# Kernel tuning notes

Measured on AMD Instinct MI355X. Metric: run time of the kernel, lower is better.

## Reference

```python
import jax, jax.numpy as jnp
import numpy as np

N = 50000      # nodes
E = 800000     # edges (avg degree 16)
D_IN = 18      # 3 fields x 6 timesteps
H = 128        # hidden_dim
HEADS = 4
DH = H // HEADS
D_OUT = 3
NEG = 0.2      # LeakyReLU slope
BN_EPS = 1e-5


def leaky(x):
    return jnp.where(x >= 0, x, NEG * x)


def segment_softmax(e, row, n):
    # numerically stable softmax over edges grouped by target node (axis 0)
    m = jax.ops.segment_max(e, row, num_segments=n)
    ex = jnp.exp(e - m[row])
    s = jax.ops.segment_sum(ex, row, num_segments=n)
    return ex / (s[row] + 1e-16)


def single_head_attn(x, row, col, Wv, b, a_src, a_dst):
    h = x @ Wv + b                                   # [N,H] values
    s_src = x @ a_src                                # [N] query scalar (dim=1)
    s_dst = x @ a_dst                                # [N] key scalar
    e = leaky(s_src[row] + s_dst[col])               # [E]
    alpha = segment_softmax(e, row, N)               # [E]
    return jax.ops.segment_sum(alpha[:, None] * h[col], row, num_segments=N)


def multi_head_attn(x, row, col, Wv, b, a_src, a_dst):
    h = jnp.einsum('nd,hde->nhe', x, Wv) + b         # [N,4,32] per-head values
    s_src = x @ a_src.T                              # [N,4] per-head Q (dim=1)
    s_dst = x @ a_dst.T                              # [N,4] per-head K (dim=1)
    e = leaky(s_src[row] + s_dst[col])               # [E,4]
    alpha = segment_softmax(e, row, N)               # [E,4]
    out = jax.ops.segment_sum(alpha[:, :, None] * h[col], row, num_segments=N)
    return out.reshape(N, HEADS * DH)                # concat heads -> [N,128]


def batch_norm_eval(x, g, bt, m, v):
    return (x - m) * jax.lax.rsqrt(v + BN_EPS) * g + bt


def setup_inputs() -> dict:
    key = jax.random.key(0)
    ks = jax.random.split(key, 16)
    rn = lambda k, shp, s=0.05: jax.random.normal(k, shp, dtype=jnp.float32) * s
    return {
        'x': rn(ks[0], (N, D_IN), 1.0),
        'edge_index': jax.random.randint(ks[1], (2, E), 0, N, dtype=jnp.int32),
        'W_in': rn(ks[2], (D_IN, H)),
        'b_in': jnp.zeros((H,), jnp.float32),
        'W_agg': rn(ks[3], (D_IN, H)),
        'b_agg': jnp.zeros((H,), jnp.float32),
        'sh_Wv': rn(ks[4], (2, H, H)),
        'sh_b': jnp.zeros((2, H), jnp.float32),
        'sh_asrc': rn(ks[5], (2, H)),
        'sh_adst': rn(ks[6], (2, H)),
        'mh_Wv': rn(ks[7], (HEADS, H, DH)),
        'mh_b': jnp.zeros((HEADS, DH), jnp.float32),
        'mh_asrc': rn(ks[8], (HEADS, H)),
        'mh_adst': rn(ks[9], (HEADS, H)),
        'bn_gamma': jnp.ones((3, H), jnp.float32),
        'bn_beta': jnp.zeros((3, H), jnp.float32),
        'bn_mean': jnp.zeros((3, H), jnp.float32),
        'bn_var': jnp.ones((3, H), jnp.float32),
        'W_o1': rn(ks[10], (H, H)),
        'b_o1': jnp.zeros((H,), jnp.float32),
        'W_o2': rn(ks[11], (H, D_OUT), 0.01),
        'b_o2': jnp.zeros((D_OUT,), jnp.float32),
    }


def reference(x, edge_index, W_in, b_in, W_agg, b_agg, sh_Wv, sh_b, sh_asrc, sh_adst,
              mh_Wv, mh_b, mh_asrc, mh_adst, bn_gamma, bn_beta, bn_mean, bn_var,
              W_o1, b_o1, W_o2, b_o2):
    row, col = edge_index[0], edge_index[1]

    # explicit neighbor mean aggregation (fused gather-scatter)
    nsum = jax.ops.segment_sum(x[col], row, num_segments=N)     # [N,D_IN]
    deg = jax.ops.segment_sum(jnp.ones((E,), x.dtype), row, num_segments=N)
    nmean = nsum / (deg[:, None] + 1e-8)

    h = (x @ W_in + b_in) + (nmean @ W_agg + b_agg)             # [N,H]
    x0 = h

    # layer 0: single-head attention + BN + residual(x0) + leaky
    h1 = single_head_attn(h, row, col, sh_Wv[0], sh_b[0], sh_asrc[0], sh_adst[0])
    h1 = batch_norm_eval(h1, bn_gamma[0], bn_beta[0], bn_mean[0], bn_var[0])
    h = leaky(x0 + h1)

    # layer 1: multi-head (4 heads, Q/K dim=1) + BN, no residual (i=1), leaky
    h2 = multi_head_attn(h, row, col, mh_Wv, mh_b, mh_asrc, mh_adst)
    h2 = batch_norm_eval(h2, bn_gamma[1], bn_beta[1], bn_mean[1], bn_var[1])
    h = leaky(h2)

    # layer 2: single-head + BN + residual + leaky
    r = h
    h3 = single_head_attn(h, row, col, sh_Wv[1], sh_b[1], sh_asrc[1], sh_adst[1])
    h3 = batch_norm_eval(h3, bn_gamma[2], bn_beta[2], bn_mean[2], bn_var[2])
    h = leaky(r + h3)

    # output head (dropout is a no-op in eval)
    delta = leaky(h @ W_o1 + b_o1) @ W_o2 + b_o2                # [N,3]

    # residual skip from last timestep of the input sequence
    return x[:, -D_OUT:] + delta
```

## Files before the change

kernel.cpp:

```cpp
#include <hip/hip_runtime.h>
#include <math.h>

#define DIN 18
#define HID 128
#define NEGS 0.2f
#define BN_EPS 1e-5f
#define SCHUNK 2048

typedef unsigned short ushort_t;
typedef __attribute__((ext_vector_type(8))) short bf16x8;
typedef __attribute__((ext_vector_type(4))) float f32x4;

__device__ __forceinline__ float leaky(float x){ return x >= 0.f ? x : NEGS * x; }

__device__ __forceinline__ float wred_sum(float v){
  #pragma unroll
  for (int off = 32; off; off >>= 1) v += __shfl_xor(v, off);
  return v;
}

__device__ __forceinline__ ushort_t f2bf(float f){
  union { float f; unsigned u; } v; v.f = f;
  unsigned r = v.u + 0x7FFFu + ((v.u >> 16) & 1u);
  return (ushort_t)(r >> 16);
}
__device__ __forceinline__ float bf_lo(unsigned p){ return __uint_as_float(p << 16); }
__device__ __forceinline__ float bf_hi(unsigned p){ return __uint_as_float(p & 0xFFFF0000u); }
__device__ __forceinline__ unsigned packbf(float a, float b){
  return (unsigned)f2bf(a) | ((unsigned)f2bf(b) << 16);
}

__device__ __forceinline__ float sel4(float v0, float v1, float v2, float v3, int hd){
  float a = (hd & 1) ? v1 : v0;
  float b = (hd & 1) ? v3 : v2;
  return (hd & 2) ? b : a;
}

__global__ void k_deg_rank(const int* __restrict__ row, int* __restrict__ deg,
                           int* __restrict__ rank, int E){
  int i = blockIdx.x * blockDim.x + threadIdx.x;
  if (i < E) rank[i] = atomicAdd(&deg[row[i]], 1);
}

__global__ void k_scan1(const int* __restrict__ deg, int* __restrict__ bsum, int n){
  __shared__ int wtot[4];
  int tid = threadIdx.x, lane = tid & 63, wid = tid >> 6;
  int base = blockIdx.x * SCHUNK + tid * 8;
  int acc = 0;
  #pragma unroll
  for (int j = 0; j < 8; ++j){
    int i = base + j;
    if (i < n) acc += deg[i];
  }
  #pragma unroll
  for (int off = 32; off; off >>= 1) acc += __shfl_xor(acc, off);
  if (lane == 0) wtot[wid] = acc;
  __syncthreads();
  if (tid == 0) bsum[blockIdx.x] = wtot[0] + wtot[1] + wtot[2] + wtot[3];
}

__global__ void k_scan2(int* __restrict__ bsum, int nb){
  int lane = threadIdx.x;
  int carry = 0;
  for (int base = 0; base < nb; base += 64){
    int i = base + lane;
    int v = (i < nb) ? bsum[i] : 0;
    #pragma unroll
    for (int off = 1; off < 64; off <<= 1){
      int u = __shfl_up(v, off);
      if (lane >= off) v += u;
    }
    if (i < nb) bsum[i] = v + carry;
    carry += __shfl(v, 63);
  }
}

__global__ void k_scan3(const int* __restrict__ deg, const int* __restrict__ bsum,
                        int* __restrict__ rowptr, int n){
  __shared__ int wtot[4];
  int tid = threadIdx.x, lane = tid & 63, wid = tid >> 6;
  int base = blockIdx.x * SCHUNK + tid * 8;
  int l[8];
  int acc = 0;
  #pragma unroll
  for (int j = 0; j < 8; ++j){
    int i = base + j;
    acc += (i < n) ? deg[i] : 0;
    l[j] = acc;
  }
  int v = acc;
  #pragma unroll
  for (int off = 1; off < 64; off <<= 1){
    int u = __shfl_up(v, off);
    if (lane >= off) v += u;
  }
  if (lane == 63) wtot[wid] = v;
  __syncthreads();
  int woff = 0;
  for (int w = 0; w < wid; ++w) woff += wtot[w];
  int boff = (blockIdx.x == 0) ? 0 : bsum[blockIdx.x - 1];
  int tpre = boff + woff + (v - acc);
  #pragma unroll
  for (int j = 0; j < 8; ++j){
    int i = base + j;
    if (i < n) rowptr[i + 1] = tpre + l[j];
  }
  if (blockIdx.x == 0 && tid == 0) rowptr[0] = 0;
}

__global__ void k_scatter(const int* __restrict__ row, const int* __restrict__ col,
                          const int* __restrict__ rowptr, const int* __restrict__ rank,
                          int* __restrict__ cols_s, int E){
  int i = blockIdx.x * blockDim.x + threadIdx.x;
  if (i < E){
    cols_s[rowptr[row[i]] + rank[i]] = col[i];
  }
}

__global__ void k_nmean(const float* __restrict__ x, const int* __restrict__ rowptr,
                        const int* __restrict__ cols, float* __restrict__ nmean, int n){
  __shared__ int s_cv[4][64];
  int wid = threadIdx.x >> 6;
  int node = blockIdx.x * 4 + wid;
  if (node >= n) return;
  int lane = threadIdx.x & 63;
  int s = rowptr[node], e = rowptr[node + 1];
  float acc = 0.f;
  for (int j0 = s; j0 < e; j0 += 64){
    int len = min(64, e - j0);
    int cv = (lane < len) ? cols[j0 + lane] : 0;
    s_cv[wid][lane] = cv;
    int k = 0;
    for (; k + 8 <= len; k += 8){
      float p[8];
      #pragma unroll
      for (int u = 0; u < 8; ++u){
        int c = s_cv[wid][k + u];
        p[u] = (lane < DIN) ? x[c * DIN + lane] : 0.f;
      }
      #pragma unroll
      for (int u = 0; u < 8; ++u) acc += p[u];
    }
    for (; k < len; ++k){
      int c = s_cv[wid][k];
      if (lane < DIN) acc += x[c * DIN + lane];
    }
  }
  if (lane < DIN){
    float d = (float)(e - s);
    nmean[node * DIN + lane] = acc / (d + 1e-8f);
  }
}

__global__ void k_h_in(const float* __restrict__ x, const float* __restrict__ nmean,
                       const float* __restrict__ Win, const float* __restrict__ bin,
                       const float* __restrict__ Wagg, const float* __restrict__ bagg,
                       const float* __restrict__ asrc, const float* __restrict__ adst,
                       float* __restrict__ ssrc, float* __restrict__ sdst,
                       ushort_t* __restrict__ out, int n){
  int wid = threadIdx.x >> 6;
  int node = blockIdx.x * 4 + wid;
  if (node >= n) return;
  int lane = threadIdx.x & 63;
  float xv = 0.f;
  if (lane < DIN) xv = x[node * DIN + lane];
  else if (lane < 2 * DIN) xv = nmean[node * DIN + (lane - DIN)];
  float acc0 = bin[lane]      + bagg[lane];
  float acc1 = bin[64 + lane] + bagg[64 + lane];
  #pragma unroll
  for (int d = 0; d < DIN; ++d){
    float xd = __shfl(xv, d);
    float nd = __shfl(xv, DIN + d);
    acc0 += xd * Win[d * HID + lane]       + nd * Wagg[d * HID + lane];
    acc1 += xd * Win[d * HID + 64 + lane]  + nd * Wagg[d * HID + 64 + lane];
  }
  out[node * HID + lane]      = f2bf(acc0);
  out[node * HID + 64 + lane] = f2bf(acc1);
  float ps = acc0 * asrc[lane] + acc1 * asrc[64 + lane];
  float pd = acc0 * adst[lane] + acc1 * adst[64 + lane];
  ps = wred_sum(ps);
  pd = wred_sum(pd);
  if (lane == 0){ ssrc[node] = ps; sdst[node] = pd; }
}

__global__ void k_wt_sh(const float* __restrict__ W, ushort_t* __restrict__ Wt){
  int i = blockIdx.x * 256 + threadIdx.x;
  int c = i >> 7, d = i & 127;
  Wt[c * HID + d] = f2bf(W[d * HID + c]);
}
__global__ void k_wt_mh(const float* __restrict__ mhWv, ushort_t* __restrict__ Wt){
  int i = blockIdx.x * 256 + threadIdx.x;
  int c = i >> 7, d = i & 127;
  Wt[c * HID + d] = f2bf(mhWv[((c >> 5) * HID + d) * 32 + (c & 31)]);
}

__global__ void k_gemm_mfma(const ushort_t* __restrict__ A, const ushort_t* __restrict__ Bt,
                            const float* __restrict__ bias, ushort_t* __restrict__ dstb,
                            int n){
  int wv = threadIdx.x >> 6, lane = threadIdx.x & 63;
  int r0 = blockIdx.x * 64 + wv * 16;
  int lr = lane & 15, lk = lane >> 4;
  int arow = r0 + lr; if (arow >= n) arow = n - 1;
  const ushort_t* Ap = A + (size_t)arow * HID + lk * 8;
  bf16x8 a[4];
  #pragma unroll
  for (int kb = 0; kb < 4; ++kb) a[kb] = *(const bf16x8*)(Ap + kb * 32);
  f32x4 acc[8];
  #pragma unroll
  for (int t = 0; t < 8; ++t) acc[t] = (f32x4){0.f, 0.f, 0.f, 0.f};
  #pragma unroll
  for (int t = 0; t < 8; ++t){
    const ushort_t* Bp = Bt + (size_t)(t * 16 + lr) * HID + lk * 8;
    #pragma unroll
    for (int kb = 0; kb < 4; ++kb){
      bf16x8 b = *(const bf16x8*)(Bp + kb * 32);
      acc[t] = __builtin_amdgcn_mfma_f32_16x16x32_bf16(a[kb], b, acc[t], 0, 0, 0);
    }
  }
  #pragma unroll
  for (int t = 0; t < 8; ++t){
    int col = t * 16 + lr;
    float bs = bias[col];
    #pragma unroll
    for (int j = 0; j < 4; ++j){
      int rr = r0 + lk * 4 + j;
      if (rr < n) dstb[(size_t)rr * HID + col] = f2bf(acc[t][j] + bs);
    }
  }
}

__global__ void k_gemm_out(const ushort_t* __restrict__ A, const ushort_t* __restrict__ Bt,
                           const float* __restrict__ bias, const float* __restrict__ Wo2,
                           const float* __restrict__ bo2, const float* __restrict__ x,
                           float* __restrict__ out, int n){
  int wv = threadIdx.x >> 6, lane = threadIdx.x & 63;
  int r0 = blockIdx.x * 64 + wv * 16;
  int lr = lane & 15, lk = lane >> 4;
  int arow = r0 + lr; if (arow >= n) arow = n - 1;
  const ushort_t* Ap = A + (size_t)arow * HID + lk * 8;
  bf16x8 a[4];
  #pragma unroll
  for (int kb = 0; kb < 4; ++kb) a[kb] = *(const bf16x8*)(Ap + kb * 32);
  f32x4 acc[8];
  #pragma unroll
  for (int t = 0; t < 8; ++t) acc[t] = (f32x4){0.f, 0.f, 0.f, 0.f};
  #pragma unroll
  for (int t = 0; t < 8; ++t){
    const ushort_t* Bp = Bt + (size_t)(t * 16 + lr) * HID + lk * 8;
    #pragma unroll
    for (int kb = 0; kb < 4; ++kb){
      bf16x8 b = *(const bf16x8*)(Bp + kb * 32);
      acc[t] = __builtin_amdgcn_mfma_f32_16x16x32_bf16(a[kb], b, acc[t], 0, 0, 0);
    }
  }
  #pragma unroll
  for (int j = 0; j < 4; ++j){
    float p0 = 0.f, p1 = 0.f, p2 = 0.f;
    #pragma unroll
    for (int t = 0; t < 8; ++t){
      int col = t * 16 + lr;
      float v = leaky(acc[t][j] + bias[col]);
      p0 += v * Wo2[col * 3 + 0];
      p1 += v * Wo2[col * 3 + 1];
      p2 += v * Wo2[col * 3 + 2];
    }
    #pragma unroll
    for (int off = 1; off < 16; off <<= 1){
      p0 += __shfl_xor(p0, off);
      p1 += __shfl_xor(p1, off);
      p2 += __shfl_xor(p2, off);
    }
    int rr = r0 + lk * 4 + j;
    if (lr == 0 && rr < n){
      out[rr * 3 + 0] = x[rr * DIN + 15] + p0 + bo2[0];
      out[rr * 3 + 1] = x[rr * DIN + 16] + p1 + bo2[1];
      out[rr * 3 + 2] = x[rr * DIN + 17] + p2 + bo2[2];
    }
  }
}

__global__ void k_agg_sh(const int* __restrict__ rowptr, const int* __restrict__ cols,
                         const float* __restrict__ ssrc, const float* __restrict__ sdst,
                         const ushort_t* __restrict__ hv, const ushort_t* __restrict__ resid,
                         const float* __restrict__ bng, const float* __restrict__ bnb,
                         const float* __restrict__ bnm, const float* __restrict__ bnv,
                         const float* __restrict__ masrc, const float* __restrict__ madst,
                         float* __restrict__ ossrc, float* __restrict__ osdst,
                         ushort_t* __restrict__ out, int n){
  __shared__ int   s_cv[4][64];
  __shared__ float s_ex[4][64];
  int wid = threadIdx.x >> 6;
  int node = blockIdx.x * 4 + wid;
  if (node >= n) return;
  int lane = threadIdx.x & 63;
  const unsigned* hv32 = (const unsigned*)hv;
  int s = rowptr[node], e = rowptr[node + 1];
  float sq = ssrc[node];
  float ssum = 0.f, a0 = 0.f, a1 = 0.f;
  for (int j0 = s; j0 < e; j0 += 64){
    int len = min(64, e - j0);
    int cv = 0; float ex = 0.f;
    if (lane < len){
      cv = cols[j0 + lane];
      ex = __expf(leaky(sq + sdst[cv]));
    }
    ssum += ex;
    s_cv[wid][lane] = cv;
    s_ex[wid][lane] = ex;
    int k = 0;
    for (; k + 16 <= len; k += 16){
      unsigned p[16]; float l[16];
      #pragma unroll
      for (int u = 0; u < 16; ++u){
        int c = s_cv[wid][k + u];
        l[u] = s_ex[wid][k + u];
        p[u] = hv32[c * 64 + lane];
      }
      #pragma unroll
      for (int u = 0; u < 16; ++u){
        a0 += l[u] * bf_lo(p[u]); a1 += l[u] * bf_hi(p[u]);
      }
    }
    for (; k + 8 <= len; k += 8){
      unsigned p[8]; float l[8];
      #pragma unroll
      for (int u = 0; u < 8; ++u){
        int c = s_cv[wid][k + u];
        l[u] = s_ex[wid][k + u];
        p[u] = hv32[c * 64 + lane];
      }
      #pragma unroll
      for (int u = 0; u < 8; ++u){
        a0 += l[u] * bf_lo(p[u]); a1 += l[u] * bf_hi(p[u]);
      }
    }
    for (; k + 4 <= len; k += 4){
      unsigned p[4]; float l[4];
      #pragma unroll
      for (int u = 0; u < 4; ++u){
        int c = s_cv[wid][k + u];
        l[u] = s_ex[wid][k + u];
        p[u] = hv32[c * 64 + lane];
      }
      #pragma unroll
      for (int u = 0; u < 4; ++u){
        a0 += l[u] * bf_lo(p[u]); a1 += l[u] * bf_hi(p[u]);
      }
    }
    for (; k < len; ++k){
      int c = s_cv[wid][k];
      float l = s_ex[wid][k];
      unsigned p = hv32[c * 64 + lane];
      a0 += l * bf_lo(p); a1 += l * bf_hi(p);
    }
  }
  ssum = wred_sum(ssum);
  float inv = 1.f / (ssum + 1e-16f);
  a0 *= inv; a1 *= inv;
  int d0 = 2 * lane, d1 = 2 * lane + 1;
  float v0 = (a0 - bnm[d0]) * rsqrtf(bnv[d0] + BN_EPS) * bng[d0] + bnb[d0];
  float v1 = (a1 - bnm[d1]) * rsqrtf(bnv[d1] + BN_EPS) * bng[d1] + bnb[d1];
  if (resid){
    unsigned rv = *(const unsigned*)&resid[node * HID + d0];
    v0 += bf_lo(rv); v1 += bf_hi(rv);
  }
  float o0 = leaky(v0), o1 = leaky(v1);
  *(unsigned*)&out[node * HID + d0] = packbf(o0, o1);
  if (ossrc){
    #pragma unroll
    for (int h = 0; h < 4; ++h){
      float ps = o0 * masrc[h * HID + d0] + o1 * masrc[h * HID + d1];
      float pd = o0 * madst[h * HID + d0] + o1 * madst[h * HID + d1];
      ps = wred_sum(ps);
      pd = wred_sum(pd);
      if (lane == 0){ ossrc[node * 4 + h] = ps; osdst[node * 4 + h] = pd; }
    }
  }
}

__global__ void k_agg_mh(const int* __restrict__ rowptr, const int* __restrict__ cols,
                         const float* __restrict__ ssrc, const float* __restrict__ sdst,
                         const ushort_t* __restrict__ hv,
                         const float* __restrict__ bng, const float* __restrict__ bnb,
                         const float* __restrict__ bnm, const float* __restrict__ bnv,
                         const float* __restrict__ sasrc, const float* __restrict__ sadst,
                         float* __restrict__ ossrc, float* __restrict__ osdst,
                         ushort_t* __restrict__ out, int n){
  __shared__ int    s_cv[4][64];
  __shared__ float4 s_ex[4][64];
  int wid = threadIdx.x >> 6;
  int node = blockIdx.x * 4 + wid;
  if (node >= n) return;
  int lane = threadIdx.x & 63;
  const unsigned* hv32 = (const unsigned*)hv;
  int s = rowptr[node], e = rowptr[node + 1];
  const float4 sq = *(const float4*)&ssrc[node * 4];
  int hd = lane >> 4;
  float s0 = 0.f, s1 = 0.f, s2 = 0.f, s3 = 0.f;
  float a0 = 0.f, a1 = 0.f;
  const float* exw = &s_ex[wid][0].x;
  for (int j0 = s; j0 < e; j0 += 64){
    int len = min(64, e - j0);
    int cv = 0;
    float e0 = 0.f, e1 = 0.f, e2 = 0.f, e3 = 0.f;
    if (lane < len){
      cv = cols[j0 + lane];
      float4 kd = *(const float4*)&sdst[cv * 4];
      e0 = __expf(leaky(sq.x + kd.x)); e1 = __expf(leaky(sq.y + kd.y));
      e2 = __expf(leaky(sq.z + kd.z)); e3 = __expf(leaky(sq.w + kd.w));
    }
    s0 += e0; s1 += e1; s2 += e2; s3 += e3;
    s_cv[wid][lane] = cv;
    s_ex[wid][lane] = make_float4(e0, e1, e2, e3);
    int k = 0;
    for (; k + 16 <= len; k += 16){
      unsigned p[16]; float l[16];
      #pragma unroll
      for (int u = 0; u < 16; ++u){
        int c = s_cv[wid][k + u];
        l[u] = exw[(k + u) * 4 + hd];
        p[u] = hv32[c * 64 + lane];
      }
      #pragma unroll
      for (int u = 0; u < 16; ++u){
        a0 += l[u] * bf_lo(p[u]); a1 += l[u] * bf_hi(p[u]);
      }
    }
    for (; k + 8 <= len; k += 8){
      unsigned p[8]; float l[8];
      #pragma unroll
      for (int u = 0; u < 8; ++u){
        int c = s_cv[wid][k + u];
        l[u] = exw[(k + u) * 4 + hd];
        p[u] = hv32[c * 64 + lane];
      }
      #pragma unroll
      for (int u = 0; u < 8; ++u){
        a0 += l[u] * bf_lo(p[u]); a1 += l[u] * bf_hi(p[u]);
      }
    }
    for (; k + 4 <= len; k += 4){
      unsigned p[4]; float l[4];
      #pragma unroll
      for (int u = 0; u < 4; ++u){
        int c = s_cv[wid][k + u];
        l[u] = exw[(k + u) * 4 + hd];
        p[u] = hv32[c * 64 + lane];
      }
      #pragma unroll
      for (int u = 0; u < 4; ++u){
        a0 += l[u] * bf_lo(p[u]); a1 += l[u] * bf_hi(p[u]);
      }
    }
    for (; k < len; ++k){
      int c = s_cv[wid][k];
      float l = exw[k * 4 + hd];
      unsigned p = hv32[c * 64 + lane];
      a0 += l * bf_lo(p); a1 += l * bf_hi(p);
    }
  }
  s0 = wred_sum(s0); s1 = wred_sum(s1);
  s2 = wred_sum(s2); s3 = wred_sum(s3);
  float i0 = 1.f / (s0 + 1e-16f), i1 = 1.f / (s1 + 1e-16f);
  float i2 = 1.f / (s2 + 1e-16f), i3 = 1.f / (s3 + 1e-16f);
  float ih = sel4(i0, i1, i2, i3, hd);
  a0 *= ih; a1 *= ih;
  int d0 = 2 * lane, d1 = 2 * lane + 1;
  float v0 = (a0 - bnm[d0]) * rsqrtf(bnv[d0] + BN_EPS) * bng[d0] + bnb[d0];
  float v1 = (a1 - bnm[d1]) * rsqrtf(bnv[d1] + BN_EPS) * bng[d1] + bnb[d1];
  float o0 = leaky(v0), o1 = leaky(v1);
  *(unsigned*)&out[node * HID + d0] = packbf(o0, o1);
  float ps = o0 * sasrc[d0] + o1 * sasrc[d1];
  float pd = o0 * sadst[d0] + o1 * sadst[d1];
  ps = wred_sum(ps);
  pd = wred_sum(pd);
  if (lane == 0){ ossrc[node] = ps; osdst[node] = pd; }
}

extern "C" void kernel_launch(void* const* d_in, const int* in_sizes, int n_in,
                              void* d_out, int out_size, void* d_ws, size_t ws_size,
                              hipStream_t stream){
  const float* x       = (const float*)d_in[0];
  const int*   ei      = (const int*)  d_in[1];
  const float* W_in    = (const float*)d_in[2];
  const float* b_in    = (const float*)d_in[3];
  const float* W_agg   = (const float*)d_in[4];
  const float* b_agg   = (const float*)d_in[5];
  const float* sh_Wv   = (const float*)d_in[6];
  const float* sh_b    = (const float*)d_in[7];
  const float* sh_asrc = (const float*)d_in[8];
  const float* sh_adst = (const float*)d_in[9];
  const float* mh_Wv   = (const float*)d_in[10];
  const float* mh_b    = (const float*)d_in[11];
  const float* mh_asrc = (const float*)d_in[12];
  const float* mh_adst = (const float*)d_in[13];
  const float* bn_g    = (const float*)d_in[14];
  const float* bn_bt   = (const float*)d_in[15];
  const float* bn_m    = (const float*)d_in[16];
  const float* bn_v    = (const float*)d_in[17];
  const float* W_o1    = (const float*)d_in[18];
  const float* b_o1    = (const float*)d_in[19];
  const float* W_o2    = (const float*)d_in[20];
  const float* b_o2    = (const float*)d_in[21];
  float* out = (float*)d_out;

  const int N = in_sizes[0] / DIN;
  const int E = in_sizes[1] / 2;
  const int* row = ei;
  const int* col = ei + E;

  char* w = (char*)d_ws;
  size_t off = 0;
  auto alloc = [&](size_t bytes) -> void* {
    void* p = w + off;
    off = (off + bytes + 255) & ~(size_t)255;
    return p;
  };
  int*      tmp    = (int*)     alloc((size_t)N * 4);
  int*      rowptr = (int*)     alloc((size_t)(N + 1) * 4);
  int*      cols_s = (int*)     alloc((size_t)E * 4);
  int*      rank   = (int*)     alloc((size_t)E * 4);
  int*      bsum   = (int*)     alloc((size_t)1024 * 4);
  float*    nmean  = (float*)   alloc((size_t)N * DIN * 4);
  float*    ssrcA  = (float*)   alloc((size_t)N * 4);
  float*    sdstA  = (float*)   alloc((size_t)N * 4);
  float*    ssrcB  = (float*)   alloc((size_t)N * 4 * 4);
  float*    sdstB  = (float*)   alloc((size_t)N * 4 * 4);
  ushort_t* wt0    = (ushort_t*)alloc((size_t)HID * HID * 2);
  ushort_t* wt1    = (ushort_t*)alloc((size_t)HID * HID * 2);
  ushort_t* wt2    = (ushort_t*)alloc((size_t)HID * HID * 2);
  ushort_t* wt3    = (ushort_t*)alloc((size_t)HID * HID * 2);
  ushort_t* b0     = (ushort_t*)alloc((size_t)N * HID * 2);
  ushort_t* b1     = (ushort_t*)alloc((size_t)N * HID * 2);
  ushort_t* hvb    = (ushort_t*)alloc((size_t)N * HID * 2);

  const int eb = (E + 255) / 256;
  const int nb4 = (N + 3) / 4;
  const int gb = (N + 63) / 64;
  const int nsb = (N + SCHUNK - 1) / SCHUNK;

  hipMemsetAsync(tmp, 0, (size_t)N * 4, stream);
  k_deg_rank<<<eb, 256, 0, stream>>>(row, tmp, rank, E);
  k_scan1<<<nsb, 256, 0, stream>>>(tmp, bsum, N);
  k_scan2<<<1, 64, 0, stream>>>(bsum, nsb);
  k_scan3<<<nsb, 256, 0, stream>>>(tmp, bsum, rowptr, N);
  k_scatter<<<eb, 256, 0, stream>>>(row, col, rowptr, rank, cols_s, E);

  k_wt_sh<<<64, 256, 0, stream>>>(sh_Wv, wt0);
  k_wt_mh<<<64, 256, 0, stream>>>(mh_Wv, wt1);
  k_wt_sh<<<64, 256, 0, stream>>>(sh_Wv + HID * HID, wt2);
  k_wt_sh<<<64, 256, 0, stream>>>(W_o1, wt3);

  k_nmean<<<nb4, 256, 0, stream>>>(x, rowptr, cols_s, nmean, N);
  k_h_in<<<nb4, 256, 0, stream>>>(x, nmean, W_in, b_in, W_agg, b_agg,
                                  sh_asrc, sh_adst, ssrcA, sdstA, b0, N);

  k_gemm_mfma<<<gb, 256, 0, stream>>>(b0, wt0, sh_b, hvb, N);
  k_agg_sh<<<nb4, 256, 0, stream>>>(rowptr, cols_s, ssrcA, sdstA, hvb, b0,
                                    bn_g, bn_bt, bn_m, bn_v,
                                    mh_asrc, mh_adst, ssrcB, sdstB, b1, N);

  k_gemm_mfma<<<gb, 256, 0, stream>>>(b1, wt1, mh_b, hvb, N);
  k_agg_mh<<<nb4, 256, 0, stream>>>(rowptr, cols_s, ssrcB, sdstB, hvb,
                                    bn_g + HID, bn_bt + HID, bn_m + HID, bn_v + HID,
                                    sh_asrc + HID, sh_adst + HID, ssrcA, sdstA, b0, N);

  k_gemm_mfma<<<gb, 256, 0, stream>>>(b0, wt2, sh_b + HID, hvb, N);
  k_agg_sh<<<nb4, 256, 0, stream>>>(rowptr, cols_s, ssrcA, sdstA, hvb, b0,
                                    bn_g + 2 * HID, bn_bt + 2 * HID, bn_m + 2 * HID, bn_v + 2 * HID,
                                    nullptr, nullptr, nullptr, nullptr, b1, N);

  k_gemm_out<<<gb, 256, 0, stream>>>(b1, wt3, b_o1, W_o2, b_o2, x, out, N);
}
```

Before: 369.2 us.

## Assign one block per node in aggregation kernels, splitting edges across waves

The neighbor-mean and attention aggregation kernels now use a whole 256-thread block per node instead of one wavefront per node. Edge indices and softmax weights are staged in shared memory, the four waves each take a strided subset of edges, and partial sums are reduced through shared memory before wave 0 applies normalization, batch norm and the projection. The aim is more memory-level parallelism per node across the random gathers. In exchange it adds block barriers, launches 50000 blocks with only about 16 edges each so most waves stay lightly loaded, and drops the unrolled batched loads.

```diff
diff --git a/kernel.cpp b/kernel.cpp
--- a/kernel.cpp
+++ b/kernel.cpp
@@ -119,36 +119,27 @@
 
 __global__ void k_nmean(const float* __restrict__ x, const int* __restrict__ rowptr,
                         const int* __restrict__ cols, float* __restrict__ nmean, int n){
-  __shared__ int s_cv[4][64];
-  int wid = threadIdx.x >> 6;
-  int node = blockIdx.x * 4 + wid;
-  if (node >= n) return;
-  int lane = threadIdx.x & 63;
+  __shared__ int   s_cv[256];
+  __shared__ float s_red[4][DIN];
+  int node = blockIdx.x;
+  int tid = threadIdx.x, w = tid >> 6, lane = tid & 63;
   int s = rowptr[node], e = rowptr[node + 1];
   float acc = 0.f;
-  for (int j0 = s; j0 < e; j0 += 64){
-    int len = min(64, e - j0);
-    int cv = (lane < len) ? cols[j0 + lane] : 0;
-    s_cv[wid][lane] = cv;
-    int k = 0;
-    for (; k + 8 <= len; k += 8){
-      float p[8];
-      #pragma unroll
-      for (int u = 0; u < 8; ++u){
-        int c = s_cv[wid][k + u];
-        p[u] = (lane < DIN) ? x[c * DIN + lane] : 0.f;
-      }
-      #pragma unroll
-      for (int u = 0; u < 8; ++u) acc += p[u];
-    }
-    for (; k < len; ++k){
-      int c = s_cv[wid][k];
-      if (lane < DIN) acc += x[c * DIN + lane];
-    }
-  }
-  if (lane < DIN){
+  for (int j0 = s; j0 < e; j0 += 256){
+    int cnt = min(256, e - j0);
+    if (tid < cnt) s_cv[tid] = cols[j0 + tid];
+    __syncthreads();
+    if (lane < DIN){
+      for (int k = w; k < cnt; k += 4) acc += x[s_cv[k] * DIN + lane];
+    }
+    __syncthreads();
+  }
+  if (lane < DIN) s_red[w][lane] = acc;
+  __syncthreads();
+  if (w == 0 && lane < DIN){
     float d = (float)(e - s);
-    nmean[node * DIN + lane] = acc / (d + 1e-8f);
+    nmean[node * DIN + lane] =
+      (s_red[0][lane] + s_red[1][lane] + s_red[2][lane] + s_red[3][lane]) / (d + 1e-8f);
   }
 }
 
@@ -287,93 +278,62 @@
                          const float* __restrict__ masrc, const float* __restrict__ madst,
                          float* __restrict__ ossrc, float* __restrict__ osdst,
                          ushort_t* __restrict__ out, int n){
-  __shared__ int   s_cv[4][64];
-  __shared__ float s_ex[4][64];
-  int wid = threadIdx.x >> 6;
-  int node = blockIdx.x * 4 + wid;
-  if (node >= n) return;
-  int lane = threadIdx.x & 63;
+  __shared__ int   s_cv[256];
+  __shared__ float s_ex[256];
+  __shared__ float s_a[4 * 128];
+  __shared__ float s_s[4];
+  int node = blockIdx.x;
+  int tid = threadIdx.x, w = tid >> 6, lane = tid & 63;
   const unsigned* hv32 = (const unsigned*)hv;
   int s = rowptr[node], e = rowptr[node + 1];
   float sq = ssrc[node];
   float ssum = 0.f, a0 = 0.f, a1 = 0.f;
-  for (int j0 = s; j0 < e; j0 += 64){
-    int len = min(64, e - j0);
-    int cv = 0; float ex = 0.f;
-    if (lane < len){
-      cv = cols[j0 + lane];
-      ex = __expf(leaky(sq + sdst[cv]));
-    }
-    ssum += ex;
-    s_cv[wid][lane] = cv;
-    s_ex[wid][lane] = ex;
-    int k = 0;
-    for (; k + 16 <= len; k += 16){
-      unsigned p[16]; float l[16];
-      #pragma unroll
-      for (int u = 0; u < 16; ++u){
-        int c = s_cv[wid][k + u];
-        l[u] = s_ex[wid][k + u];
-        p[u] = hv32[c * 64 + lane];
-      }
-      #pragma unroll
-      for (int u = 0; u < 16; ++u){
-        a0 += l[u] * bf_lo(p[u]); a1 += l[u] * bf_hi(p[u]);
-      }
-    }
-    for (; k + 8 <= len; k += 8){
-      unsigned p[8]; float l[8];
-      #pragma unroll
-      for (int u = 0; u < 8; ++u){
-        int c = s_cv[wid][k + u];
-        l[u] = s_ex[wid][k + u];
-        p[u] = hv32[c * 64 + lane];
-      }
-      #pragma unroll
-      for (int u = 0; u < 8; ++u){
-        a0 += l[u] * bf_lo(p[u]); a1 += l[u] * bf_hi(p[u]);
-      }
-    }
-    for (; k + 4 <= len; k += 4){
-      unsigned p[4]; float l[4];
-      #pragma unroll
-      for (int u = 0; u < 4; ++u){
-        int c = s_cv[wid][k + u];
-        l[u] = s_ex[wid][k + u];
-        p[u] = hv32[c * 64 + lane];
-      }
-      #pragma unroll
-      for (int u = 0; u < 4; ++u){
-        a0 += l[u] * bf_lo(p[u]); a1 += l[u] * bf_hi(p[u]);
-      }
-    }
-    for (; k < len; ++k){
-      int c = s_cv[wid][k];
-      float l = s_ex[wid][k];
+  for (int j0 = s; j0 < e; j0 += 256){
+    int cnt = min(256, e - j0);
+    if (tid < cnt){
+      int cv = cols[j0 + tid];
+      float ex = __expf(leaky(sq + sdst[cv]));
+      ssum += ex;
+      s_cv[tid] = cv;
+      s_ex[tid] = ex;
+    }
+    __syncthreads();
+    for (int k = w; k < cnt; k += 4){
+      int c = s_cv[k]; float l = s_ex[k];
       unsigned p = hv32[c * 64 + lane];
       a0 += l * bf_lo(p); a1 += l * bf_hi(p);
     }
+    __syncthreads();
   }
   ssum = wred_sum(ssum);
-  float inv = 1.f / (ssum + 1e-16f);
-  a0 *= inv; a1 *= inv;
-  int d0 = 2 * lane, d1 = 2 * lane + 1;
-  float v0 = (a0 - bnm[d0]) * rsqrtf(bnv[d0] + BN_EPS) * bng[d0] + bnb[d0];
-  float v1 = (a1 - bnm[d1]) * rsqrtf(bnv[d1] + BN_EPS) * bng[d1] + bnb[d1];
-  if (resid){
-    unsigned rv = *(const unsigned*)&resid[node * HID + d0];
-    v0 += bf_lo(rv); v1 += bf_hi(rv);
-  }
-  float o0 = leaky(v0), o1 = leaky(v1);
-  *(unsigned*)&out[node * HID + d0] = packbf(o0, o1);
-  if (ossrc){
-    #pragma unroll
-    for (int h = 0; h < 4; ++h){
-      float ps = o0 * masrc[h * HID + d0] + o1 * masrc[h * HID + d1];
-      float pd = o0 * madst[h * HID + d0] + o1 * madst[h * HID + d1];
-      ps = wred_sum(ps);
-      pd = wred_sum(pd);
-      if (lane == 0){ ossrc[node * 4 + h] = ps; osdst[node * 4 + h] = pd; }
+  if (lane == 0) s_s[w] = ssum;
+  s_a[w * 128 + lane]      = a0;
+  s_a[w * 128 + 64 + lane] = a1;
+  __syncthreads();
+  if (w == 0){
+    float tot = s_s[0] + s_s[1] + s_s[2] + s_s[3];
+    a0 = s_a[lane]      + s_a[128 + lane]      + s_a[256 + lane]      + s_a[384 + lane];
+    a1 = s_a[64 + lane] + s_a[128 + 64 + lane] + s_a[256 + 64 + lane] + s_a[384 + 64 + lane];
+    float inv = 1.f / (tot + 1e-16f);
+    a0 *= inv; a1 *= inv;
+    int d0 = 2 * lane, d1 = 2 * lane + 1;
+    float v0 = (a0 - bnm[d0]) * rsqrtf(bnv[d0] + BN_EPS) * bng[d0] + bnb[d0];
+    float v1 = (a1 - bnm[d1]) * rsqrtf(bnv[d1] + BN_EPS) * bng[d1] + bnb[d1];
+    if (resid){
+      unsigned rv = *(const unsigned*)&resid[node * HID + d0];
+      v0 += bf_lo(rv); v1 += bf_hi(rv);
+    }
+    float o0 = leaky(v0), o1 = leaky(v1);
+    *(unsigned*)&out[node * HID + d0] = packbf(o0, o1);
+    if (ossrc){
+      #pragma unroll
+      for (int h = 0; h < 4; ++h){
+        float ps = o0 * masrc[h * HID + d0] + o1 * masrc[h * HID + d1];
+        float pd = o0 * madst[h * HID + d0] + o1 * madst[h * HID + d1];
+        ps = wred_sum(ps);
+        pd = wred_sum(pd);
+        if (lane == 0){ ossrc[node * 4 + h] = ps; osdst[node * 4 + h] = pd; }
+      }
     }
   }
 }
@@ -386,95 +346,67 @@
                          const float* __restrict__ sasrc, const float* __restrict__ sadst,
                          float* __restrict__ ossrc, float* __restrict__ osdst,
                          ushort_t* __restrict__ out, int n){
-  __shared__ int    s_cv[4][64];
-  __shared__ float4 s_ex[4][64];
-  int wid = threadIdx.x >> 6;
-  int node = blockIdx.x * 4 + wid;
-  if (node >= n) return;
-  int lane = threadIdx.x & 63;
+  __shared__ int    s_cv[256];
+  __shared__ float4 s_ex[256];
+  __shared__ float  s_a[4 * 128];
+  __shared__ float  s_s[4][4];
+  int node = blockIdx.x;
+  int tid = threadIdx.x, w = tid >> 6, lane = tid & 63;
   const unsigned* hv32 = (const unsigned*)hv;
   int s = rowptr[node], e = rowptr[node + 1];
   const float4 sq = *(const float4*)&ssrc[node * 4];
   int hd = lane >> 4;
-  float s0 = 0.f, s1 = 0.f, s2 = 0.f, s3 = 0.f;
+  float ss0 = 0.f, ss1 = 0.f, ss2 = 0.f, ss3 = 0.f;
   float a0 = 0.f, a1 = 0.f;
-  const float* exw = &s_ex[wid][0].x;
-  for (int j0 = s; j0 < e; j0 += 64){
-    int len = min(64, e - j0);
-    int cv = 0;
-    float e0 = 0.f, e1 = 0.f, e2 = 0.f, e3 = 0.f;
-    if (lane < len){
-      cv = cols[j0 + lane];
+  const float* exw = &s_ex[0].x;
+  for (int j0 = s; j0 < e; j0 += 256){
+    int cnt = min(256, e - j0);
+    if (tid < cnt){
+      int cv = cols[j0 + tid];
       float4 kd = *(const float4*)&sdst[cv * 4];
-      e0 = __expf(leaky(sq.x + kd.x)); e1 = __expf(leaky(sq.y + kd.y));
-      e2 = __expf(leaky(sq.z + kd.z)); e3 = __expf(leaky(sq.w + kd.w));
-    }
-    s0 += e0; s1 += e1; s2 += e2; s3 += e3;
-    s_cv[wid][lane] = cv;
-    s_ex[wid][lane] = make_float4(e0, e1, e2, e3);
-    int k = 0;
-    for (; k + 16 <= len; k += 16){
-      unsigned p[16]; float l[16];
-      #pragma unroll
-      for (int u = 0; u < 16; ++u){
-        int c = s_cv[wid][k + u];
-        l[u] = exw[(k + u) * 4 + hd];
-        p[u] = hv32[c * 64 + lane];
-      }
-      #pragma unroll
-      for (int u = 0; u < 16; ++u){
-        a0 += l[u] * bf_lo(p[u]); a1 += l[u] * bf_hi(p[u]);
-      }
-    }
-    for (; k + 8 <= len; k += 8){
-      unsigned p[8]; float l[8];
-      #pragma unroll
-      for (int u = 0; u < 8; ++u){
-        int c = s_cv[wid][k + u];
-        l[u] = exw[(k + u) * 4 + hd];
-        p[u] = hv32[c * 64 + lane];
-      }
-      #pragma unroll
-      for (int u = 0; u < 8; ++u){
-        a0 += l[u] * bf_lo(p[u]); a1 += l[u] * bf_hi(p[u]);
-      }
-    }
-    for (; k + 4 <= len; k += 4){
-      unsigned p[4]; float l[4];
-      #pragma unroll
-      for (int u = 0; u < 4; ++u){
-        int c = s_cv[wid][k + u];
-        l[u] = exw[(k + u) * 4 + hd];
-        p[u] = hv32[c * 64 + lane];
-      }
-      #pragma unroll
-      for (int u = 0; u < 4; ++u){
-        a0 += l[u] * bf_lo(p[u]); a1 += l[u] * bf_hi(p[u]);
-      }
-    }
-    for (; k < len; ++k){
-      int c = s_cv[wid][k];
+      float e0 = __expf(leaky(sq.x + kd.x)), e1 = __expf(leaky(sq.y + kd.y));
+      float e2 = __expf(leaky(sq.z + kd.z)), e3 = __expf(leaky(sq.w + kd.w));
+      ss0 += e0; ss1 += e1; ss2 += e2; ss3 += e3;
+      s_cv[tid] = cv;
+      s_ex[tid] = make_float4(e0, e1, e2, e3);
+    }
+    __syncthreads();
+    for (int k = w; k < cnt; k += 4){
+      int c = s_cv[k];
       float l = exw[k * 4 + hd];
       unsigned p = hv32[c * 64 + lane];
       a0 += l * bf_lo(p); a1 += l * bf_hi(p);
     }
-  }
-  s0 = wred_sum(s0); s1 = wred_sum(s1);
-  s2 = wred_sum(s2); s3 = wred_sum(s3);
-  float i0 = 1.f / (s0 + 1e-16f), i1 = 1.f / (s1 + 1e-16f);
-  float i2 = 1.f / (s2 + 1e-16f), i3 = 1.f / (s3 + 1e-16f);
-  float ih = sel4(i0, i1, i2, i3, hd);
-  a0 *= ih; a1 *= ih;
-  int d0 = 2 * lane, d1 = 2 * lane + 1;
-  float v0 = (a0 - bnm[d0]) * rsqrtf(bnv[d0] + BN_EPS) * bng[d0] + bnb[d0];
-  float v1 = (a1 - bnm[d1]) * rsqrtf(bnv[d1] + BN_EPS) * bng[d1] + bnb[d1];
-  float o0 = leaky(v0), o1 = leaky(v1);
-  *(unsigned*)&out[node * HID + d0] = packbf(o0, o1);
-  float ps = o0 * sasrc[d0] + o1 * sasrc[d1];
-  float pd = o0 * sadst[d0] + o1 * sadst[d1];
-  ps = wred_sum(ps);
-  pd = wred_sum(pd);
-  if (lane == 0){ ossrc[node] = ps; osdst[node] = pd; }
+    __syncthreads();
+  }
+  ss0 = wred_sum(ss0); ss1 = wred_sum(ss1);
+  ss2 = wred_sum(ss2); ss3 = wred_sum(ss3);
+  if (lane == 0){ s_s[w][0] = ss0; s_s[w][1] = ss1; s_s[w][2] = ss2; s_s[w][3] = ss3; }
+  s_a[w * 128 + lane]      = a0;
+  s_a[w * 128 + 64 + lane] = a1;
+  __syncthreads();
+  if (w == 0){
+    float t0 = s_s[0][0] + s_s[1][0] + s_s[2][0] + s_s[3][0];
+    float t1 = s_s[0][1] + s_s[1][1] + s_s[2][1] + s_s[3][1];
+    float t2 = s_s[0][2] + s_s[1][2] + s_s[2][2] + s_s[3][2];
+    float t3 = s_s[0][3] + s_s[1][3] + s_s[2][3] + s_s[3][3];
+    a0 = s_a[lane]      + s_a[128 + lane]      + s_a[256 + lane]      + s_a[384 + lane];
+    a1 = s_a[64 + lane] + s_a[128 + 64 + lane] + s_a[256 + 64 + lane] + s_a[384 + 64 + lane];
+    float i0 = 1.f / (t0 + 1e-16f), i1 = 1.f / (t1 + 1e-16f);
+    float i2 = 1.f / (t2 + 1e-16f), i3 = 1.f / (t3 + 1e-16f);
+    float ih = sel4(i0, i1, i2, i3, hd);
+    a0 *= ih; a1 *= ih;
+    int d0 = 2 * lane, d1 = 2 * lane + 1;
+    float v0 = (a0 - bnm[d0]) * rsqrtf(bnv[d0] + BN_EPS) * bng[d0] + bnb[d0];
+    float v1 = (a1 - bnm[d1]) * rsqrtf(bnv[d1] + BN_EPS) * bng[d1] + bnb[d1];
+    float o0 = leaky(v0), o1 = leaky(v1);
+    *(unsigned*)&out[node * HID + d0] = packbf(o0, o1);
+    float ps = o0 * sasrc[d0] + o1 * sasrc[d1];
+    float pd = o0 * sadst[d0] + o1 * sadst[d1];
+    ps = wred_sum(ps);
+    pd = wred_sum(pd);
+    if (lane == 0){ ossrc[node] = ps; osdst[node] = pd; }
+  }
 }
 
 extern "C" void kernel_launch(void* const* d_in, const int* in_sizes, int n_in,
@@ -551,24 +483,24 @@
   k_wt_sh<<<64, 256, 0, stream>>>(sh_Wv + HID * HID, wt2);
   k_wt_sh<<<64, 256, 0, stream>>>(W_o1, wt3);
 
-  k_nmean<<<nb4, 256, 0, stream>>>(x, rowptr, cols_s, nmean, N);
+  k_nmean<<<N, 256, 0, stream>>>(x, rowptr, cols_s, nmean, N);
   k_h_in<<<nb4, 256, 0, stream>>>(x, nmean, W_in, b_in, W_agg, b_agg,
                                   sh_asrc, sh_adst, ssrcA, sdstA, b0, N);
 
   k_gemm_mfma<<<gb, 256, 0, stream>>>(b0, wt0, sh_b, hvb, N);
-  k_agg_sh<<<nb4, 256, 0, stream>>>(rowptr, cols_s, ssrcA, sdstA, hvb, b0,
-                                    bn_g, bn_bt, bn_m, bn_v,
-                                    mh_asrc, mh_adst, ssrcB, sdstB, b1, N);
+  k_agg_sh<<<N, 256, 0, stream>>>(rowptr, cols_s, ssrcA, sdstA, hvb, b0,
+                                  bn_g, bn_bt, bn_m, bn_v,
+                                  mh_asrc, mh_adst, ssrcB, sdstB, b1, N);
 
   k_gemm_mfma<<<gb, 256, 0, stream>>>(b1, wt1, mh_b, hvb, N);
-  k_agg_mh<<<nb4, 256, 0, stream>>>(rowptr, cols_s, ssrcB, sdstB, hvb,
-                                    bn_g + HID, bn_bt + HID, bn_m + HID, bn_v + HID,
-                                    sh_asrc + HID, sh_adst + HID, ssrcA, sdstA, b0, N);
+  k_agg_mh<<<N, 256, 0, stream>>>(rowptr, cols_s, ssrcB, sdstB, hvb,
+                                  bn_g + HID, bn_bt + HID, bn_m + HID, bn_v + HID,
+                                  sh_asrc + HID, sh_adst + HID, ssrcA, sdstA, b0, N);
 
   k_gemm_mfma<<<gb, 256, 0, stream>>>(b0, wt2, sh_b + HID, hvb, N);
-  k_agg_sh<<<nb4, 256, 0, stream>>>(rowptr, cols_s, ssrcA, sdstA, hvb, b0,
-                                    bn_g + 2 * HID, bn_bt + 2 * HID, bn_m + 2 * HID, bn_v + 2 * HID,
-                                    nullptr, nullptr, nullptr, nullptr, b1, N);
+  k_agg_sh<<<N, 256, 0, stream>>>(rowptr, cols_s, ssrcA, sdstA, hvb, b0,
+                                  bn_g + 2 * HID, bn_bt + 2 * HID, bn_m + 2 * HID, bn_v + 2 * HID,
+                                  nullptr, nullptr, nullptr, nullptr, b1, N);
 
   k_gemm_out<<<gb, 256, 0, stream>>>(b1, wt3, b_o1, W_o2, b_o2, x, out, N);
 }
```

After: 542.1 us. 1.47x slower.
